# Optimization experiments

Hardware: AMD Instinct MI355X
Metric: run time of the kernel (lower is better)

The kernel has to match this reference:

```python
import jax, jax.numpy as jnp
import numpy as np

ASSIGN_RATIO = 0.1  # hard-coded inside coarsen_graph in the original
EPS_CUT = 1e-7
EPS_NORM = 1e-12  # torch F.normalize eps


def _normalize_batch_adj(adj):
    # adj: [B, N, N]
    n = adj.shape[1]
    A = adj + jnp.eye(n, dtype=adj.dtype)
    deg_inv_sqrt = jnp.clip(A.sum(-1), 1.0, None) ** -0.5  # [B, N]
    newA = deg_inv_sqrt[..., :, None] * A * deg_inv_sqrt[..., None, :]
    row_mask = (adj.sum(-1) > 0).astype(adj.dtype)  # [B, N]
    return row_mask[..., :, None] * newA


def setup_inputs():
    key = jax.random.key(0)
    k0, k1, k2, k3, k4 = jax.random.split(key, 5)
    B, N, D, T = 512, 128, 256, 512
    concept_hidden = jax.random.normal(k0, (B, N, D), jnp.float32)
    adj = jax.random.uniform(k1, (B, N, N), jnp.float32)
    head = jax.random.randint(k2, (B, T), 0, N)
    lin_w = jax.random.normal(k3, (1, D), jnp.float32) / np.sqrt(D).astype(np.float32)
    bias = jax.random.normal(k4, (1,), jnp.float32)
    return {"concept_hidden": concept_hidden, "adj": adj, "head": head,
            "lin_w": lin_w, "bias": bias}


def reference(concept_hidden, adj, head, lin_w, bias):
    # concept_hidden: [B, N, D], adj: [B, N, N], head: [B, T] node indices
    x = concept_hidden
    B, N, D = x.shape

    out = x @ lin_w.T                      # [B, N, 1]  self.lin(x)
    norm_adj = _normalize_batch_adj(adj)   # [B, N, N]
    out = norm_adj @ out + bias            # [B, N, 1]
    alpha = jax.nn.sigmoid(out ** 2)[..., 0]  # [B, N]

    # batch_num_nodes[i] = len(set(head[i]))  -> count unique via sort
    hs = jnp.sort(head, axis=-1)
    n_uniq = 1 + (hs[:, 1:] != hs[:, :-1]).sum(-1)  # [B]

    # per-sample k = ceil(n * 0.1) + 1 (only when n > 1); cut = k-th largest alpha
    k = jnp.ceil(n_uniq.astype(jnp.float32) * ASSIGN_RATIO).astype(jnp.int32) + 1
    a_desc = jnp.sort(alpha, axis=-1)[:, ::-1]       # descending
    idx = jnp.clip(k - 1, 0, N - 1)
    cut = jnp.take_along_axis(a_desc, idx[:, None], axis=-1)[:, 0]
    cut = jnp.where(n_uniq > 1, cut, jnp.zeros_like(cut))  # [B]

    cut_alpha = jax.nn.relu(alpha + EPS_CUT - cut[:, None])  # [B, N]

    # S = norm_adj * cut_alpha broadcast over rows, then L1-normalize rows
    S = norm_adj * cut_alpha[:, None, :]
    S = S / jnp.clip(jnp.abs(S).sum(-1, keepdims=True), EPS_NORM, None)

    St = jnp.swapaxes(S, 1, 2)             # [B, N, N]
    embedding_tensor = St @ x              # S^T x   [B, N, D]
    new_adj = (St @ adj) @ S               # S^T A S [B, N, N]
    return embedding_tensor, new_adj
```

## Files before the change

kernel.cpp:

```cpp
#include <hip/hip_runtime.h>

#define Bsz 512
#define Nn  128
#define Dd  256
#define Tt  512

typedef __attribute__((ext_vector_type(8))) short short8;
typedef __attribute__((ext_vector_type(4))) float f32x4;

__device__ __forceinline__ ushort f2bf(float f) {
    union { float f; unsigned u; } v; v.f = f;
    unsigned r = v.u + 0x7fffu + ((v.u >> 16) & 1u);
    return (ushort)(r >> 16);
}
__device__ __forceinline__ unsigned pk2(float a, float b) {
    return (unsigned)f2bf(a) | ((unsigned)f2bf(b) << 16);
}

__global__ __launch_bounds__(256) void xprep(
    const float* __restrict__ x, const float* __restrict__ lin_w,
    float* __restrict__ dotv2, ushort* __restrict__ xT)
{
    const int h = blockIdx.x, b = blockIdx.y;
    __shared__ float xbufT[32][130];
    __shared__ float pdot[128][8];
    __shared__ float wS[128];
    const int t = threadIdx.x;
    if (t < 128) wS[t] = lin_w[h * 128 + t];
    const int c4 = t & 7;
    const int kb = t >> 3;
    const int kc = t & 15, dsub = t >> 4;
    float p[4] = {0.f, 0.f, 0.f, 0.f};
    __syncthreads();

    for (int c = 0; c < 4; ++c) {
        const int dl = 4 * c4;
        float4 v[4];
#pragma unroll
        for (int i = 0; i < 4; ++i)
            v[i] = *(const float4*)&x[((size_t)b * Nn + (kb + 32 * i)) * Dd
                                      + h * 128 + c * 32 + dl];
        const float w0 = wS[c*32+dl],   w1 = wS[c*32+dl+1];
        const float w2 = wS[c*32+dl+2], w3 = wS[c*32+dl+3];
#pragma unroll
        for (int i = 0; i < 4; ++i) {
            p[i] += v[i].x*w0 + v[i].y*w1 + v[i].z*w2 + v[i].w*w3;
            xbufT[dl    ][kb + 32*i] = v[i].x;
            xbufT[dl + 1][kb + 32*i] = v[i].y;
            xbufT[dl + 2][kb + 32*i] = v[i].z;
            xbufT[dl + 3][kb + 32*i] = v[i].w;
        }
        __syncthreads();
#pragma unroll
        for (int pp = 0; pp < 2; ++pp) {
            int d = dsub + 16 * pp;
            float2 q0 = *(float2*)&xbufT[d][kc*8 + 0];
            float2 q1 = *(float2*)&xbufT[d][kc*8 + 2];
            float2 q2 = *(float2*)&xbufT[d][kc*8 + 4];
            float2 q3 = *(float2*)&xbufT[d][kc*8 + 6];
            uint4 pkv;
            pkv.x = pk2(q0.x, q0.y);
            pkv.y = pk2(q1.x, q1.y);
            pkv.z = pk2(q2.x, q2.y);
            pkv.w = pk2(q3.x, q3.y);
            *(uint4*)&xT[((size_t)b * Dd + h * 128 + c * 32 + d) * Nn + kc * 8] = pkv;
        }
        __syncthreads();
    }
#pragma unroll
    for (int i = 0; i < 4; ++i) pdot[kb + 32*i][c4] = p[i];
    __syncthreads();
    if (t < 128) {
        float s = 0.f;
#pragma unroll
        for (int j = 0; j < 8; ++j) s += pdot[t][j];
        dotv2[((size_t)b * Nn + t) * 2 + h] = s;
    }
}

__global__ __launch_bounds__(256) void sprep(
    const float* __restrict__ adj, const int* __restrict__ head,
    const float* __restrict__ dotv2, const float* __restrict__ bias,
    ushort* __restrict__ STbf)
{
    const int b = blockIdx.x;
    __shared__ __align__(16) float adjS[Nn][132];
    __shared__ __align__(16) float ttS[Nn], disS[Nn], maskS[Nn],
                                   alphaS[Nn], uS[Nn], rowcS[Nn];
    __shared__ float partS[Nn][2];
    __shared__ int   flags[Nn];
    __shared__ int   nuniq_s;
    __shared__ float cut_s;

    const int t = threadIdx.x;
    const float bias0 = bias[0];
    if (t < Nn) flags[t] = 0;
    if (t == 0) { nuniq_s = 0; cut_s = 0.f; }

    const float* adjb = adj + (size_t)b * (Nn * Nn);
#pragma unroll
    for (int i = 0; i < 16; ++i) {
        int f = t + 256 * i;
        int rr = f >> 5, c = (f & 31) * 4;
        *(float4*)&adjS[rr][c] = *(const float4*)&adjb[rr * Nn + c];
    }
    __syncthreads();

    {
        int h0 = head[(size_t)b * Tt + t];
        int h1 = head[(size_t)b * Tt + 256 + t];
        flags[h0] = 1; flags[h1] = 1;
    }

    const int r = t >> 1, hh = t & 1, base = hh * 64;
    {
        float4 s4 = {0.f, 0.f, 0.f, 0.f};
#pragma unroll
        for (int j = 0; j < 16; ++j) {
            float4 v = *(float4*)&adjS[r][base + 4*j];
            s4.x += v.x; s4.y += v.y; s4.z += v.z; s4.w += v.w;
        }
        partS[r][hh] = (s4.x + s4.y) + (s4.z + s4.w);
    }
    __syncthreads();
    if (t < Nn) {
        float rs  = partS[t][0] + partS[t][1];
        float m   = (rs > 0.f) ? 1.f : 0.f;
        float dis = 1.f / sqrtf(fmaxf(rs + 1.f, 1.f));
        maskS[t] = m; disS[t] = dis;
        float lin = dotv2[((size_t)b * Nn + t) * 2]
                  + dotv2[((size_t)b * Nn + t) * 2 + 1];
        ttS[t] = dis * lin;
        atomicAdd(&nuniq_s, flags[t]);
    }
    __syncthreads();
    {
        float4 a = {0.f, 0.f, 0.f, 0.f};
#pragma unroll
        for (int j = 0; j < 16; ++j) {
            float4 v = *(float4*)&adjS[r][base + 4*j];
            float4 w = *(float4*)&ttS[base + 4*j];
            a.x += v.x*w.x; a.y += v.y*w.y; a.z += v.z*w.z; a.w += v.w*w.w;
        }
        partS[r][hh] = (a.x + a.y) + (a.z + a.w);
    }
    __syncthreads();
    if (t < Nn) {
        float mv = partS[t][0] + partS[t][1];
        float o  = maskS[t] * disS[t] * (mv + ttS[t]) + bias0;
        alphaS[t] = 1.f / (1.f + expf(-o * o));
    }
    __syncthreads();
    if (t < Nn) {
        int nu = nuniq_s;
        if (nu > 1) {
            int idx = (int)ceilf((float)nu * 0.1f);
            if (idx > Nn - 1) idx = Nn - 1;
            float an = alphaS[t];
            int cg = 0, ce = 0;
            for (int j = 0; j < Nn; ++j) {
                float aj = alphaS[j];
                cg += (aj > an); ce += (aj == an);
            }
            if (cg <= idx && idx < cg + ce) cut_s = an;
        }
    }
    __syncthreads();
    if (t < Nn) uS[t] = fmaxf(alphaS[t] + 1e-7f - cut_s, 0.f) * disS[t];
    __syncthreads();
    {
        float4 a = {0.f, 0.f, 0.f, 0.f};
#pragma unroll
        for (int j = 0; j < 16; ++j) {
            float4 v = *(float4*)&adjS[r][base + 4*j];
            float4 w = *(float4*)&uS[base + 4*j];
            a.x += v.x*w.x; a.y += v.y*w.y; a.z += v.z*w.z; a.w += v.w*w.w;
        }
        partS[r][hh] = (a.x + a.y) + (a.z + a.w);
    }
    __syncthreads();
    if (t < Nn) {
        float tot  = partS[t][0] + partS[t][1] + uS[t];
        float rsum = maskS[t] * disS[t] * tot;
        rowcS[t] = maskS[t] * disS[t] / fmaxf(rsum, 1e-12f);
    }
    __syncthreads();
    {
        const float um = uS[r];
        ushort* outp = STbf + ((size_t)b * Nn + r) * Nn + base;
#pragma unroll
        for (int kcc = 0; kcc < 8; ++kcc) {
            int k0 = base + kcc * 8;
            float vv[8];
#pragma unroll
            for (int j = 0; j < 8; ++j) {
                int k = k0 + j;
                vv[j] = rowcS[k] * (adjS[k][r] + ((k == r) ? 1.f : 0.f)) * um;
            }
            uint4 pkv;
            pkv.x = pk2(vv[0], vv[1]); pkv.y = pk2(vv[2], vv[3]);
            pkv.z = pk2(vv[4], vv[5]); pkv.w = pk2(vv[6], vv[7]);
            *(uint4*)(outp + kcc * 8) = pkv;
        }
    }
}

__global__ __launch_bounds__(256, 2) void emb_gemm(
    const ushort* __restrict__ STbf, const ushort* __restrict__ xT,
    float* __restrict__ emb)
{
    const int d0 = blockIdx.x * 128;
    const int b  = blockIdx.y;
    __shared__ ushort STl[128][136];
    __shared__ ushort xTl[128][136];
    const int t = threadIdx.x;
    const uint4* sg = (const uint4*)(STbf + (size_t)b * Nn * Nn);
    const uint4* xg = (const uint4*)(xT + ((size_t)b * Dd + d0) * Nn);
#pragma unroll
    for (int i = 0; i < 8; ++i) {
        int f = t + 256 * i;
        int row = f >> 4, c8 = f & 15;
        *(uint4*)&STl[row][c8 * 8] = sg[f];
        *(uint4*)&xTl[row][c8 * 8] = xg[f];
    }
    __syncthreads();

    const int lane = t & 63, wv = t >> 6;
    const int l15 = lane & 15, quad = lane >> 4;
    const int m0 = wv * 32;
    f32x4 acc[2][8];
#pragma unroll
    for (int mt = 0; mt < 2; ++mt)
#pragma unroll
        for (int nt = 0; nt < 8; ++nt) acc[mt][nt] = (f32x4){0.f, 0.f, 0.f, 0.f};

#pragma unroll
    for (int k0 = 0; k0 < 128; k0 += 32) {
        short8 a0 = *(const short8*)&STl[m0 + l15][k0 + quad * 8];
        short8 a1 = *(const short8*)&STl[m0 + 16 + l15][k0 + quad * 8];
        short8 bf[8];
#pragma unroll
        for (int nt = 0; nt < 8; ++nt)
            bf[nt] = *(const short8*)&xTl[nt * 16 + l15][k0 + quad * 8];
#pragma unroll
        for (int nt = 0; nt < 8; ++nt) {
            acc[0][nt] = __builtin_amdgcn_mfma_f32_16x16x32_bf16(a0, bf[nt], acc[0][nt], 0, 0, 0);
            acc[1][nt] = __builtin_amdgcn_mfma_f32_16x16x32_bf16(a1, bf[nt], acc[1][nt], 0, 0, 0);
        }
    }
#pragma unroll
    for (int mt = 0; mt < 2; ++mt)
#pragma unroll
        for (int nt = 0; nt < 8; ++nt)
#pragma unroll
            for (int rr = 0; rr < 4; ++rr) {
                int row = m0 + mt * 16 + quad * 4 + rr;
                int col = d0 + nt * 16 + l15;
                emb[((size_t)b * Nn + row) * Dd + col] = acc[mt][nt][rr];
            }
}

__global__ __launch_bounds__(256, 2) void padj_gemm(
    const float* __restrict__ adj, const ushort* __restrict__ STbf,
    float* __restrict__ nadj)
{
    const int b = blockIdx.x;
    __shared__ ushort bufA[128][136];
    __shared__ ushort STl[128][136];
    const int t = threadIdx.x;

    const float* adjb = adj + (size_t)b * Nn * Nn;
#pragma unroll
    for (int i = 0; i < 16; ++i) {
        int f = t + 256 * i;
        int rr = f >> 5, c4 = f & 31;
        float4 v = *(const float4*)&adjb[rr * Nn + c4 * 4];
        uint2 w; w.x = pk2(v.x, v.y); w.y = pk2(v.z, v.w);
        *(uint2*)&bufA[rr][c4 * 4] = w;
    }
    const uint4* sg = (const uint4*)(STbf + (size_t)b * Nn * Nn);
#pragma unroll
    for (int i = 0; i < 8; ++i) {
        int f = t + 256 * i;
        *(uint4*)&STl[f >> 4][(f & 15) * 8] = sg[f];
    }
    __syncthreads();

    const int lane = t & 63, wv = t >> 6;
    const int l15 = lane & 15, quad = lane >> 4;
    const int m0 = wv * 32;
    f32x4 acc[2][8];
#pragma unroll
    for (int mt = 0; mt < 2; ++mt)
#pragma unroll
        for (int nt = 0; nt < 8; ++nt) acc[mt][nt] = (f32x4){0.f, 0.f, 0.f, 0.f};

#pragma unroll
    for (int k0 = 0; k0 < 128; k0 += 32) {
        short8 a0 = *(const short8*)&bufA[m0 + l15][k0 + quad * 8];
        short8 a1 = *(const short8*)&bufA[m0 + 16 + l15][k0 + quad * 8];
        short8 bf[8];
#pragma unroll
        for (int nt = 0; nt < 8; ++nt)
            bf[nt] = *(const short8*)&STl[nt * 16 + l15][k0 + quad * 8];
#pragma unroll
        for (int nt = 0; nt < 8; ++nt) {
            acc[0][nt] = __builtin_amdgcn_mfma_f32_16x16x32_bf16(a0, bf[nt], acc[0][nt], 0, 0, 0);
            acc[1][nt] = __builtin_amdgcn_mfma_f32_16x16x32_bf16(a1, bf[nt], acc[1][nt], 0, 0, 0);
        }
    }
    __syncthreads();
#pragma unroll
    for (int mt = 0; mt < 2; ++mt)
#pragma unroll
        for (int nt = 0; nt < 8; ++nt) {
            int j    = nt * 16 + l15;
            int mcol = m0 + mt * 16 + quad * 4;
            uint2 w;
            w.x = pk2(acc[mt][nt][0], acc[mt][nt][1]);
            w.y = pk2(acc[mt][nt][2], acc[mt][nt][3]);
            *(uint2*)&bufA[j][mcol] = w;
        }
    __syncthreads();

#pragma unroll
    for (int mt = 0; mt < 2; ++mt)
#pragma unroll
        for (int nt = 0; nt < 8; ++nt) acc[mt][nt] = (f32x4){0.f, 0.f, 0.f, 0.f};

#pragma unroll
    for (int k0 = 0; k0 < 128; k0 += 32) {
        short8 a0 = *(const short8*)&STl[m0 + l15][k0 + quad * 8];
        short8 a1 = *(const short8*)&STl[m0 + 16 + l15][k0 + quad * 8];
        short8 bf[8];
#pragma unroll
        for (int nt = 0; nt < 8; ++nt)
            bf[nt] = *(const short8*)&bufA[nt * 16 + l15][k0 + quad * 8];
#pragma unroll
        for (int nt = 0; nt < 8; ++nt) {
            acc[0][nt] = __builtin_amdgcn_mfma_f32_16x16x32_bf16(a0, bf[nt], acc[0][nt], 0, 0, 0);
            acc[1][nt] = __builtin_amdgcn_mfma_f32_16x16x32_bf16(a1, bf[nt], acc[1][nt], 0, 0, 0);
        }
    }
#pragma unroll
    for (int mt = 0; mt < 2; ++mt)
#pragma unroll
        for (int nt = 0; nt < 8; ++nt)
#pragma unroll
            for (int rr = 0; rr < 4; ++rr) {
                int row = m0 + mt * 16 + quad * 4 + rr;
                int col = nt * 16 + l15;
                nadj[((size_t)b * Nn + row) * Nn + col] = acc[mt][nt][rr];
            }
}

extern "C" void kernel_launch(void* const* d_in, const int* in_sizes, int n_in,
                              void* d_out, int out_size, void* d_ws, size_t ws_size,
                              hipStream_t stream)
{
    const float* x     = (const float*)d_in[0];
    const float* adj   = (const float*)d_in[1];
    const int*   head  = (const int*)d_in[2];
    const float* lin_w = (const float*)d_in[3];
    const float* bias  = (const float*)d_in[4];

    float* emb  = (float*)d_out;
    float* nadj = emb + (size_t)Bsz * Nn * Dd;

    ushort* STbf = (ushort*)d_ws;
    ushort* xT   = STbf + (size_t)Bsz * Nn * Nn;
    float*  dotv2 = (float*)(xT + (size_t)Bsz * Dd * Nn);

    xprep<<<dim3(2, Bsz), 256, 0, stream>>>(x, lin_w, dotv2, xT);
    sprep<<<Bsz, 256, 0, stream>>>(adj, head, dotv2, bias, STbf);
    emb_gemm<<<dim3(2, Bsz), 256, 0, stream>>>(STbf, xT, emb);
    padj_gemm<<<Bsz, 256, 0, stream>>>(adj, STbf, nadj);
}
```

Baseline: 230.6 us.

## Split S construction across more blocks and merge the two GEMM kernels

The monolithic per-sample sprep kernel is split up. Degree and mask row sums move into the x-prep launch as extra blocks. A lighter alphacut kernel reads adj from global memory instead of staging a 64KB shared tile, and a build_st kernel builds S^T with 4 blocks per sample. The embedding and S^T A S GEMMs are merged into one launch with role-selected blocks. The aim is higher occupancy and parallelism in the S-preparation stage, which previously ran one heavy-LDS block per sample. The cost is extra global round-trips for intermediates and adj being re-read several times.

```diff
diff --git a/kernel.cpp b/kernel.cpp
--- a/kernel.cpp
+++ b/kernel.cpp
@@ -17,142 +17,143 @@
     return (unsigned)f2bf(a) | ((unsigned)f2bf(b) << 16);
 }
 
-__global__ __launch_bounds__(256) void xprep(
-    const float* __restrict__ x, const float* __restrict__ lin_w,
-    float* __restrict__ dotv2, ushort* __restrict__ xT)
-{
-    const int h = blockIdx.x, b = blockIdx.y;
+__global__ __launch_bounds__(256) void prep1(
+    const float* __restrict__ x, const float* __restrict__ adj,
+    const float* __restrict__ lin_w,
+    float* __restrict__ dotv2, ushort* __restrict__ xT,
+    float* __restrict__ disG, float* __restrict__ maskG)
+{
+    const int bx = blockIdx.x, b = blockIdx.y;
+    const int t = threadIdx.x;
     __shared__ float xbufT[32][130];
     __shared__ float pdot[128][8];
     __shared__ float wS[128];
-    const int t = threadIdx.x;
-    if (t < 128) wS[t] = lin_w[h * 128 + t];
-    const int c4 = t & 7;
-    const int kb = t >> 3;
-    const int kc = t & 15, dsub = t >> 4;
-    float p[4] = {0.f, 0.f, 0.f, 0.f};
-    __syncthreads();
-
-    for (int c = 0; c < 4; ++c) {
-        const int dl = 4 * c4;
-        float4 v[4];
-#pragma unroll
-        for (int i = 0; i < 4; ++i)
-            v[i] = *(const float4*)&x[((size_t)b * Nn + (kb + 32 * i)) * Dd
-                                      + h * 128 + c * 32 + dl];
-        const float w0 = wS[c*32+dl],   w1 = wS[c*32+dl+1];
-        const float w2 = wS[c*32+dl+2], w3 = wS[c*32+dl+3];
-#pragma unroll
-        for (int i = 0; i < 4; ++i) {
-            p[i] += v[i].x*w0 + v[i].y*w1 + v[i].z*w2 + v[i].w*w3;
-            xbufT[dl    ][kb + 32*i] = v[i].x;
-            xbufT[dl + 1][kb + 32*i] = v[i].y;
-            xbufT[dl + 2][kb + 32*i] = v[i].z;
-            xbufT[dl + 3][kb + 32*i] = v[i].w;
-        }
-        __syncthreads();
-#pragma unroll
-        for (int pp = 0; pp < 2; ++pp) {
-            int d = dsub + 16 * pp;
-            float2 q0 = *(float2*)&xbufT[d][kc*8 + 0];
-            float2 q1 = *(float2*)&xbufT[d][kc*8 + 2];
-            float2 q2 = *(float2*)&xbufT[d][kc*8 + 4];
-            float2 q3 = *(float2*)&xbufT[d][kc*8 + 6];
-            uint4 pkv;
-            pkv.x = pk2(q0.x, q0.y);
-            pkv.y = pk2(q1.x, q1.y);
-            pkv.z = pk2(q2.x, q2.y);
-            pkv.w = pk2(q3.x, q3.y);
-            *(uint4*)&xT[((size_t)b * Dd + h * 128 + c * 32 + d) * Nn + kc * 8] = pkv;
-        }
-        __syncthreads();
-    }
-#pragma unroll
-    for (int i = 0; i < 4; ++i) pdot[kb + 32*i][c4] = p[i];
-    __syncthreads();
+    __shared__ float red[32][8];
+
+    if (bx < 2) {
+        const int h = bx;
+        if (t < 128) wS[t] = lin_w[h * 128 + t];
+        const int c4 = t & 7;
+        const int kb = t >> 3;
+        const int kc = t & 15, dsub = t >> 4;
+        float p[4] = {0.f, 0.f, 0.f, 0.f};
+        __syncthreads();
+        for (int c = 0; c < 4; ++c) {
+            const int dl = 4 * c4;
+            float4 v[4];
+#pragma unroll
+            for (int i = 0; i < 4; ++i)
+                v[i] = *(const float4*)&x[((size_t)b * Nn + (kb + 32 * i)) * Dd
+                                          + h * 128 + c * 32 + dl];
+            const float w0 = wS[c*32+dl],   w1 = wS[c*32+dl+1];
+            const float w2 = wS[c*32+dl+2], w3 = wS[c*32+dl+3];
+#pragma unroll
+            for (int i = 0; i < 4; ++i) {
+                p[i] += v[i].x*w0 + v[i].y*w1 + v[i].z*w2 + v[i].w*w3;
+                xbufT[dl    ][kb + 32*i] = v[i].x;
+                xbufT[dl + 1][kb + 32*i] = v[i].y;
+                xbufT[dl + 2][kb + 32*i] = v[i].z;
+                xbufT[dl + 3][kb + 32*i] = v[i].w;
+            }
+            __syncthreads();
+#pragma unroll
+            for (int pp = 0; pp < 2; ++pp) {
+                int d = dsub + 16 * pp;
+                float2 q0 = *(float2*)&xbufT[d][kc*8 + 0];
+                float2 q1 = *(float2*)&xbufT[d][kc*8 + 2];
+                float2 q2 = *(float2*)&xbufT[d][kc*8 + 4];
+                float2 q3 = *(float2*)&xbufT[d][kc*8 + 6];
+                uint4 pkv;
+                pkv.x = pk2(q0.x, q0.y);
+                pkv.y = pk2(q1.x, q1.y);
+                pkv.z = pk2(q2.x, q2.y);
+                pkv.w = pk2(q3.x, q3.y);
+                *(uint4*)&xT[((size_t)b * Dd + h * 128 + c * 32 + d) * Nn + kc * 8] = pkv;
+            }
+            __syncthreads();
+        }
+#pragma unroll
+        for (int i = 0; i < 4; ++i) pdot[kb + 32*i][c4] = p[i];
+        __syncthreads();
+        if (t < 128) {
+            float s = 0.f;
+#pragma unroll
+            for (int j = 0; j < 8; ++j) s += pdot[t][j];
+            dotv2[((size_t)b * Nn + t) * 2 + h] = s;
+        }
+    } else {
+        const int g = bx - 2;
+        const int r0 = g * 32;
+        const int row = r0 + (t >> 3), sub = t & 7;
+        const float* rp = adj + (size_t)b * Nn * Nn + (size_t)row * Nn + sub * 4;
+        float4 a4 = {0.f, 0.f, 0.f, 0.f};
+#pragma unroll
+        for (int j = 0; j < 4; ++j) {
+            float4 v = *(const float4*)(rp + j * 32);
+            a4.x += v.x; a4.y += v.y; a4.z += v.z; a4.w += v.w;
+        }
+        red[t >> 3][sub] = (a4.x + a4.y) + (a4.z + a4.w);
+        __syncthreads();
+        if (t < 32) {
+            float s = 0.f;
+#pragma unroll
+            for (int j = 0; j < 8; ++j) s += red[t][j];
+            maskG[(size_t)b * Nn + r0 + t] = (s > 0.f) ? 1.f : 0.f;
+            disG[(size_t)b * Nn + r0 + t]  = 1.f / sqrtf(fmaxf(s + 1.f, 1.f));
+        }
+    }
+}
+
+__global__ __launch_bounds__(256) void alphacut(
+    const float* __restrict__ adj, const int* __restrict__ head,
+    const float* __restrict__ dotv2, const float* __restrict__ disG,
+    const float* __restrict__ maskG, const float* __restrict__ bias,
+    float* __restrict__ uG, float* __restrict__ rowcG)
+{
+    const int b = blockIdx.x, t = threadIdx.x;
+    __shared__ float ttS[128], disS[128], maskS[128], alphaS[128], uS[128];
+    __shared__ float partS[128][2];
+    __shared__ int   flags[128];
+    __shared__ int   nuniq;
+    __shared__ float cutS;
+    const float bias0 = bias[0];
+
+    if (t < 128) flags[t] = 0;
+    if (t == 0) { nuniq = 0; cutS = 0.f; }
+    __syncthreads();
+    { int h0 = head[(size_t)b * Tt + t];
+      int h1 = head[(size_t)b * Tt + 256 + t];
+      flags[h0] = 1; flags[h1] = 1; }
     if (t < 128) {
-        float s = 0.f;
-#pragma unroll
-        for (int j = 0; j < 8; ++j) s += pdot[t][j];
-        dotv2[((size_t)b * Nn + t) * 2 + h] = s;
-    }
-}
-
-__global__ __launch_bounds__(256) void sprep(
-    const float* __restrict__ adj, const int* __restrict__ head,
-    const float* __restrict__ dotv2, const float* __restrict__ bias,
-    ushort* __restrict__ STbf)
-{
-    const int b = blockIdx.x;
-    __shared__ __align__(16) float adjS[Nn][132];
-    __shared__ __align__(16) float ttS[Nn], disS[Nn], maskS[Nn],
-                                   alphaS[Nn], uS[Nn], rowcS[Nn];
-    __shared__ float partS[Nn][2];
-    __shared__ int   flags[Nn];
-    __shared__ int   nuniq_s;
-    __shared__ float cut_s;
-
-    const int t = threadIdx.x;
-    const float bias0 = bias[0];
-    if (t < Nn) flags[t] = 0;
-    if (t == 0) { nuniq_s = 0; cut_s = 0.f; }
-
-    const float* adjb = adj + (size_t)b * (Nn * Nn);
-#pragma unroll
-    for (int i = 0; i < 16; ++i) {
-        int f = t + 256 * i;
-        int rr = f >> 5, c = (f & 31) * 4;
-        *(float4*)&adjS[rr][c] = *(const float4*)&adjb[rr * Nn + c];
-    }
-    __syncthreads();
-
-    {
-        int h0 = head[(size_t)b * Tt + t];
-        int h1 = head[(size_t)b * Tt + 256 + t];
-        flags[h0] = 1; flags[h1] = 1;
-    }
-
-    const int r = t >> 1, hh = t & 1, base = hh * 64;
-    {
-        float4 s4 = {0.f, 0.f, 0.f, 0.f};
-#pragma unroll
-        for (int j = 0; j < 16; ++j) {
-            float4 v = *(float4*)&adjS[r][base + 4*j];
-            s4.x += v.x; s4.y += v.y; s4.z += v.z; s4.w += v.w;
-        }
-        partS[r][hh] = (s4.x + s4.y) + (s4.z + s4.w);
-    }
-    __syncthreads();
-    if (t < Nn) {
-        float rs  = partS[t][0] + partS[t][1];
-        float m   = (rs > 0.f) ? 1.f : 0.f;
-        float dis = 1.f / sqrtf(fmaxf(rs + 1.f, 1.f));
-        maskS[t] = m; disS[t] = dis;
-        float lin = dotv2[((size_t)b * Nn + t) * 2]
-                  + dotv2[((size_t)b * Nn + t) * 2 + 1];
-        ttS[t] = dis * lin;
-        atomicAdd(&nuniq_s, flags[t]);
-    }
-    __syncthreads();
+        float d = disG[(size_t)b * Nn + t];
+        disS[t] = d; maskS[t] = maskG[(size_t)b * Nn + t];
+        ttS[t] = d * (dotv2[((size_t)b * Nn + t) * 2]
+                    + dotv2[((size_t)b * Nn + t) * 2 + 1]);
+    }
+    __syncthreads();
+    if (t < 128) atomicAdd(&nuniq, flags[t]);
+
+    const float* adjb = adj + (size_t)b * Nn * Nn;
+    const int r = t >> 1, hh = t & 1, cb = hh * 64;
     {
         float4 a = {0.f, 0.f, 0.f, 0.f};
 #pragma unroll
         for (int j = 0; j < 16; ++j) {
-            float4 v = *(float4*)&adjS[r][base + 4*j];
-            float4 w = *(float4*)&ttS[base + 4*j];
+            float4 v = *(const float4*)&adjb[(size_t)r * Nn + cb + 4*j];
+            float4 w = *(float4*)&ttS[cb + 4*j];
             a.x += v.x*w.x; a.y += v.y*w.y; a.z += v.z*w.z; a.w += v.w*w.w;
         }
         partS[r][hh] = (a.x + a.y) + (a.z + a.w);
     }
     __syncthreads();
-    if (t < Nn) {
+    if (t < 128) {
         float mv = partS[t][0] + partS[t][1];
         float o  = maskS[t] * disS[t] * (mv + ttS[t]) + bias0;
         alphaS[t] = 1.f / (1.f + expf(-o * o));
     }
     __syncthreads();
-    if (t < Nn) {
-        int nu = nuniq_s;
+    if (t < 128) {
+        int nu = nuniq;
         if (nu > 1) {
             int idx = (int)ceilf((float)nu * 0.1f);
             if (idx > Nn - 1) idx = Nn - 1;
@@ -162,66 +163,111 @@
                 float aj = alphaS[j];
                 cg += (aj > an); ce += (aj == an);
             }
-            if (cg <= idx && idx < cg + ce) cut_s = an;
-        }
-    }
-    __syncthreads();
-    if (t < Nn) uS[t] = fmaxf(alphaS[t] + 1e-7f - cut_s, 0.f) * disS[t];
+            if (cg <= idx && idx < cg + ce) cutS = an;
+        }
+    }
+    __syncthreads();
+    if (t < 128) uS[t] = fmaxf(alphaS[t] + 1e-7f - cutS, 0.f) * disS[t];
     __syncthreads();
     {
         float4 a = {0.f, 0.f, 0.f, 0.f};
 #pragma unroll
         for (int j = 0; j < 16; ++j) {
-            float4 v = *(float4*)&adjS[r][base + 4*j];
-            float4 w = *(float4*)&uS[base + 4*j];
+            float4 v = *(const float4*)&adjb[(size_t)r * Nn + cb + 4*j];
+            float4 w = *(float4*)&uS[cb + 4*j];
             a.x += v.x*w.x; a.y += v.y*w.y; a.z += v.z*w.z; a.w += v.w*w.w;
         }
         partS[r][hh] = (a.x + a.y) + (a.z + a.w);
     }
     __syncthreads();
-    if (t < Nn) {
+    if (t < 128) {
         float tot  = partS[t][0] + partS[t][1] + uS[t];
         float rsum = maskS[t] * disS[t] * tot;
-        rowcS[t] = maskS[t] * disS[t] / fmaxf(rsum, 1e-12f);
-    }
-    __syncthreads();
-    {
-        const float um = uS[r];
-        ushort* outp = STbf + ((size_t)b * Nn + r) * Nn + base;
-#pragma unroll
-        for (int kcc = 0; kcc < 8; ++kcc) {
-            int k0 = base + kcc * 8;
-            float vv[8];
-#pragma unroll
-            for (int j = 0; j < 8; ++j) {
-                int k = k0 + j;
-                vv[j] = rowcS[k] * (adjS[k][r] + ((k == r) ? 1.f : 0.f)) * um;
-            }
-            uint4 pkv;
-            pkv.x = pk2(vv[0], vv[1]); pkv.y = pk2(vv[2], vv[3]);
-            pkv.z = pk2(vv[4], vv[5]); pkv.w = pk2(vv[6], vv[7]);
-            *(uint4*)(outp + kcc * 8) = pkv;
-        }
-    }
-}
-
-__global__ __launch_bounds__(256, 2) void emb_gemm(
-    const ushort* __restrict__ STbf, const ushort* __restrict__ xT,
-    float* __restrict__ emb)
-{
-    const int d0 = blockIdx.x * 128;
-    const int b  = blockIdx.y;
-    __shared__ ushort STl[128][136];
-    __shared__ ushort xTl[128][136];
+        rowcG[(size_t)b * Nn + t] = maskS[t] * disS[t] / fmaxf(rsum, 1e-12f);
+        uG[(size_t)b * Nn + t]    = uS[t];
+    }
+}
+
+__global__ __launch_bounds__(256) void build_st(
+    const float* __restrict__ adj, const float* __restrict__ uG,
+    const float* __restrict__ rowcG, ushort* __restrict__ STbf)
+{
+    const int g = blockIdx.x, b = blockIdx.y, t = threadIdx.x;
+    const int m0 = g * 32;
+    __shared__ float slabT[32][132];
+    __shared__ float rowcS[128];
+    __shared__ float uS[32];
+
+    if (t < 128) rowcS[t] = rowcG[(size_t)b * Nn + t];
+    if (t < 32)  uS[t]    = uG[(size_t)b * Nn + m0 + t];
+
+    const float* adjb = adj + (size_t)b * Nn * Nn;
+#pragma unroll
+    for (int i = 0; i < 4; ++i) {
+        int f = t + 256 * i;
+        int k = f >> 3, cc = (f & 7) * 4;
+        float4 v = *(const float4*)&adjb[(size_t)k * Nn + m0 + cc];
+        slabT[cc    ][k] = v.x; slabT[cc + 1][k] = v.y;
+        slabT[cc + 2][k] = v.z; slabT[cc + 3][k] = v.w;
+    }
+    __syncthreads();
+
+    const int mloc = t >> 3, m = m0 + mloc;
+    const int ks   = (t & 7) * 16;
+    const float um = uS[mloc];
+    float vv[16];
+#pragma unroll
+    for (int q = 0; q < 4; ++q) {
+        float4 a = *(float4*)&slabT[mloc][ks + 4 * q];
+        int k = ks + 4 * q;
+        vv[4*q    ] = rowcS[k    ] * (a.x + ((k     == m) ? 1.f : 0.f)) * um;
+        vv[4*q + 1] = rowcS[k + 1] * (a.y + ((k + 1 == m) ? 1.f : 0.f)) * um;
+        vv[4*q + 2] = rowcS[k + 2] * (a.z + ((k + 2 == m) ? 1.f : 0.f)) * um;
+        vv[4*q + 3] = rowcS[k + 3] * (a.w + ((k + 3 == m) ? 1.f : 0.f)) * um;
+    }
+    uint4 p0, p1;
+    p0.x = pk2(vv[0],  vv[1]);  p0.y = pk2(vv[2],  vv[3]);
+    p0.z = pk2(vv[4],  vv[5]);  p0.w = pk2(vv[6],  vv[7]);
+    p1.x = pk2(vv[8],  vv[9]);  p1.y = pk2(vv[10], vv[11]);
+    p1.z = pk2(vv[12], vv[13]); p1.w = pk2(vv[14], vv[15]);
+    ushort* outp = STbf + ((size_t)b * Nn + m) * Nn + ks;
+    *(uint4*)outp       = p0;
+    *(uint4*)(outp + 8) = p1;
+}
+
+__global__ __launch_bounds__(256, 2) void gemm3(
+    const float* __restrict__ adj, const ushort* __restrict__ STbf,
+    const ushort* __restrict__ xT, float* __restrict__ emb,
+    float* __restrict__ nadj)
+{
+    const int role = blockIdx.x, b = blockIdx.y;
+    __shared__ ushort bufB[128][136];
+    __shared__ ushort bufS[128][136];
     const int t = threadIdx.x;
+
     const uint4* sg = (const uint4*)(STbf + (size_t)b * Nn * Nn);
-    const uint4* xg = (const uint4*)(xT + ((size_t)b * Dd + d0) * Nn);
 #pragma unroll
     for (int i = 0; i < 8; ++i) {
         int f = t + 256 * i;
-        int row = f >> 4, c8 = f & 15;
-        *(uint4*)&STl[row][c8 * 8] = sg[f];
-        *(uint4*)&xTl[row][c8 * 8] = xg[f];
+        *(uint4*)&bufS[f >> 4][(f & 15) * 8] = sg[f];
+    }
+    if (role < 2) {
+        const uint4* xg = (const uint4*)(xT + ((size_t)b * Dd + role * 128) * Nn);
+#pragma unroll
+        for (int i = 0; i < 8; ++i) {
+            int f = t + 256 * i;
+            *(uint4*)&bufB[f >> 4][(f & 15) * 8] = xg[f];
+        }
+    } else {
+        const float* adjb = adj + (size_t)b * Nn * Nn;
+#pragma unroll
+        for (int i = 0; i < 16; ++i) {
+            int f = t + 256 * i;
+            int rr = f >> 5, c4 = f & 31;
+            float4 v = *(const float4*)&adjb[(size_t)rr * Nn + c4 * 4];
+            uint2 w; w.x = pk2(v.x, v.y); w.y = pk2(v.z, v.w);
+            *(uint2*)&bufB[rr][c4 * 4] = w;
+        }
     }
     __syncthreads();
 
@@ -234,124 +280,89 @@
 #pragma unroll
         for (int nt = 0; nt < 8; ++nt) acc[mt][nt] = (f32x4){0.f, 0.f, 0.f, 0.f};
 
-#pragma unroll
-    for (int k0 = 0; k0 < 128; k0 += 32) {
-        short8 a0 = *(const short8*)&STl[m0 + l15][k0 + quad * 8];
-        short8 a1 = *(const short8*)&STl[m0 + 16 + l15][k0 + quad * 8];
-        short8 bf[8];
-#pragma unroll
-        for (int nt = 0; nt < 8; ++nt)
-            bf[nt] = *(const short8*)&xTl[nt * 16 + l15][k0 + quad * 8];
-#pragma unroll
-        for (int nt = 0; nt < 8; ++nt) {
-            acc[0][nt] = __builtin_amdgcn_mfma_f32_16x16x32_bf16(a0, bf[nt], acc[0][nt], 0, 0, 0);
-            acc[1][nt] = __builtin_amdgcn_mfma_f32_16x16x32_bf16(a1, bf[nt], acc[1][nt], 0, 0, 0);
-        }
-    }
-#pragma unroll
-    for (int mt = 0; mt < 2; ++mt)
-#pragma unroll
-        for (int nt = 0; nt < 8; ++nt)
-#pragma unroll
-            for (int rr = 0; rr < 4; ++rr) {
-                int row = m0 + mt * 16 + quad * 4 + rr;
-                int col = d0 + nt * 16 + l15;
-                emb[((size_t)b * Nn + row) * Dd + col] = acc[mt][nt][rr];
-            }
-}
-
-__global__ __launch_bounds__(256, 2) void padj_gemm(
-    const float* __restrict__ adj, const ushort* __restrict__ STbf,
-    float* __restrict__ nadj)
-{
-    const int b = blockIdx.x;
-    __shared__ ushort bufA[128][136];
-    __shared__ ushort STl[128][136];
-    const int t = threadIdx.x;
-
-    const float* adjb = adj + (size_t)b * Nn * Nn;
-#pragma unroll
-    for (int i = 0; i < 16; ++i) {
-        int f = t + 256 * i;
-        int rr = f >> 5, c4 = f & 31;
-        float4 v = *(const float4*)&adjb[rr * Nn + c4 * 4];
-        uint2 w; w.x = pk2(v.x, v.y); w.y = pk2(v.z, v.w);
-        *(uint2*)&bufA[rr][c4 * 4] = w;
-    }
-    const uint4* sg = (const uint4*)(STbf + (size_t)b * Nn * Nn);
-#pragma unroll
-    for (int i = 0; i < 8; ++i) {
-        int f = t + 256 * i;
-        *(uint4*)&STl[f >> 4][(f & 15) * 8] = sg[f];
-    }
-    __syncthreads();
-
-    const int lane = t & 63, wv = t >> 6;
-    const int l15 = lane & 15, quad = lane >> 4;
-    const int m0 = wv * 32;
-    f32x4 acc[2][8];
-#pragma unroll
-    for (int mt = 0; mt < 2; ++mt)
-#pragma unroll
-        for (int nt = 0; nt < 8; ++nt) acc[mt][nt] = (f32x4){0.f, 0.f, 0.f, 0.f};
-
-#pragma unroll
-    for (int k0 = 0; k0 < 128; k0 += 32) {
-        short8 a0 = *(const short8*)&bufA[m0 + l15][k0 + quad * 8];
-        short8 a1 = *(const short8*)&bufA[m0 + 16 + l15][k0 + quad * 8];
-        short8 bf[8];
-#pragma unroll
-        for (int nt = 0; nt < 8; ++nt)
-            bf[nt] = *(const short8*)&STl[nt * 16 + l15][k0 + quad * 8];
-#pragma unroll
-        for (int nt = 0; nt < 8; ++nt) {
-            acc[0][nt] = __builtin_amdgcn_mfma_f32_16x16x32_bf16(a0, bf[nt], acc[0][nt], 0, 0, 0);
-            acc[1][nt] = __builtin_amdgcn_mfma_f32_16x16x32_bf16(a1, bf[nt], acc[1][nt], 0, 0, 0);
-        }
-    }
-    __syncthreads();
-#pragma unroll
-    for (int mt = 0; mt < 2; ++mt)
-#pragma unroll
-        for (int nt = 0; nt < 8; ++nt) {
-            int j    = nt * 16 + l15;
-            int mcol = m0 + mt * 16 + quad * 4;
-            uint2 w;
-            w.x = pk2(acc[mt][nt][0], acc[mt][nt][1]);
-            w.y = pk2(acc[mt][nt][2], acc[mt][nt][3]);
-            *(uint2*)&bufA[j][mcol] = w;
-        }
-    __syncthreads();
-
-#pragma unroll
-    for (int mt = 0; mt < 2; ++mt)
-#pragma unroll
-        for (int nt = 0; nt < 8; ++nt) acc[mt][nt] = (f32x4){0.f, 0.f, 0.f, 0.f};
-
-#pragma unroll
-    for (int k0 = 0; k0 < 128; k0 += 32) {
-        short8 a0 = *(const short8*)&STl[m0 + l15][k0 + quad * 8];
-        short8 a1 = *(const short8*)&STl[m0 + 16 + l15][k0 + quad * 8];
-        short8 bf[8];
-#pragma unroll
-        for (int nt = 0; nt < 8; ++nt)
-            bf[nt] = *(const short8*)&bufA[nt * 16 + l15][k0 + quad * 8];
-#pragma unroll
-        for (int nt = 0; nt < 8; ++nt) {
-            acc[0][nt] = __builtin_amdgcn_mfma_f32_16x16x32_bf16(a0, bf[nt], acc[0][nt], 0, 0, 0);
-            acc[1][nt] = __builtin_amdgcn_mfma_f32_16x16x32_bf16(a1, bf[nt], acc[1][nt], 0, 0, 0);
-        }
-    }
-#pragma unroll
-    for (int mt = 0; mt < 2; ++mt)
-#pragma unroll
-        for (int nt = 0; nt < 8; ++nt)
-#pragma unroll
-            for (int rr = 0; rr < 4; ++rr) {
-                int row = m0 + mt * 16 + quad * 4 + rr;
-                int col = nt * 16 + l15;
-                nadj[((size_t)b * Nn + row) * Nn + col] = acc[mt][nt][rr];
-            }
+    if (role < 2) {
+#pragma unroll
+        for (int k0 = 0; k0 < 128; k0 += 32) {
+            short8 a0 = *(const short8*)&bufS[m0 + l15][k0 + quad * 8];
+            short8 a1 = *(const short8*)&bufS[m0 + 16 + l15][k0 + quad * 8];
+            short8 bf[8];
+#pragma unroll
+            for (int nt = 0; nt < 8; ++nt)
+                bf[nt] = *(const short8*)&bufB[nt * 16 + l15][k0 + quad * 8];
+#pragma unroll
+            for (int nt = 0; nt < 8; ++nt) {
+                acc[0][nt] = __builtin_amdgcn_mfma_f32_16x16x32_bf16(a0, bf[nt], acc[0][nt], 0, 0, 0);
+                acc[1][nt] = __builtin_amdgcn_mfma_f32_16x16x32_bf16(a1, bf[nt], acc[1][nt], 0, 0, 0);
+            }
+        }
+        const int d0 = role * 128;
+#pragma unroll
+        for (int mt = 0; mt < 2; ++mt)
+#pragma unroll
+            for (int nt = 0; nt < 8; ++nt)
+#pragma unroll
+                for (int rr = 0; rr < 4; ++rr) {
+                    int row = m0 + mt * 16 + quad * 4 + rr;
+                    int col = d0 + nt * 16 + l15;
+                    emb[((size_t)b * Nn + row) * Dd + col] = acc[mt][nt][rr];
+                }
+    } else {
+#pragma unroll
+        for (int k0 = 0; k0 < 128; k0 += 32) {
+            short8 a0 = *(const short8*)&bufB[m0 + l15][k0 + quad * 8];
+            short8 a1 = *(const short8*)&bufB[m0 + 16 + l15][k0 + quad * 8];
+            short8 bf[8];
+#pragma unroll
+            for (int nt = 0; nt < 8; ++nt)
+                bf[nt] = *(const short8*)&bufS[nt * 16 + l15][k0 + quad * 8];
+#pragma unroll
+            for (int nt = 0; nt < 8; ++nt) {
+                acc[0][nt] = __builtin_amdgcn_mfma_f32_16x16x32_bf16(a0, bf[nt], acc[0][nt], 0, 0, 0);
+                acc[1][nt] = __builtin_amdgcn_mfma_f32_16x16x32_bf16(a1, bf[nt], acc[1][nt], 0, 0, 0);
+            }
+        }
+        __syncthreads();
+#pragma unroll
+        for (int mt = 0; mt < 2; ++mt)
+#pragma unroll
+            for (int nt = 0; nt < 8; ++nt) {
+                int j    = nt * 16 + l15;
+                int mcol = m0 + mt * 16 + quad * 4;
+                uint2 w;
+                w.x = pk2(acc[mt][nt][0], acc[mt][nt][1]);
+                w.y = pk2(acc[mt][nt][2], acc[mt][nt][3]);
+                *(uint2*)&bufB[j][mcol] = w;
+            }
+        __syncthreads();
+#pragma unroll
+        for (int mt = 0; mt < 2; ++mt)
+#pragma unroll
+            for (int nt = 0; nt < 8; ++nt) acc[mt][nt] = (f32x4){0.f, 0.f, 0.f, 0.f};
+#pragma unroll
+        for (int k0 = 0; k0 < 128; k0 += 32) {
+            short8 a0 = *(const short8*)&bufS[m0 + l15][k0 + quad * 8];
+            short8 a1 = *(const short8*)&bufS[m0 + 16 + l15][k0 + quad * 8];
+            short8 bf[8];
+#pragma unroll
+            for (int nt = 0; nt < 8; ++nt)
+                bf[nt] = *(const short8*)&bufB[nt * 16 + l15][k0 + quad * 8];
+#pragma unroll
+            for (int nt = 0; nt < 8; ++nt) {
+                acc[0][nt] = __builtin_amdgcn_mfma_f32_16x16x32_bf16(a0, bf[nt], acc[0][nt], 0, 0, 0);
+                acc[1][nt] = __builtin_amdgcn_mfma_f32_16x16x32_bf16(a1, bf[nt], acc[1][nt], 0, 0, 0);
+            }
+        }
+#pragma unroll
+        for (int mt = 0; mt < 2; ++mt)
+#pragma unroll
+            for (int nt = 0; nt < 8; ++nt)
+#pragma unroll
+                for (int rr = 0; rr < 4; ++rr) {
+                    int row = m0 + mt * 16 + quad * 4 + rr;
+                    int col = nt * 16 + l15;
+                    nadj[((size_t)b * Nn + row) * Nn + col] = acc[mt][nt][rr];
+                }
+    }
 }
 
 extern "C" void kernel_launch(void* const* d_in, const int* in_sizes, int n_in,
@@ -367,12 +378,16 @@
     float* emb  = (float*)d_out;
     float* nadj = emb + (size_t)Bsz * Nn * Dd;
 
-    ushort* STbf = (ushort*)d_ws;
-    ushort* xT   = STbf + (size_t)Bsz * Nn * Nn;
+    ushort* STbf  = (ushort*)d_ws;
+    ushort* xT    = STbf + (size_t)Bsz * Nn * Nn;
     float*  dotv2 = (float*)(xT + (size_t)Bsz * Dd * Nn);
-
-    xprep<<<dim3(2, Bsz), 256, 0, stream>>>(x, lin_w, dotv2, xT);
-    sprep<<<Bsz, 256, 0, stream>>>(adj, head, dotv2, bias, STbf);
-    emb_gemm<<<dim3(2, Bsz), 256, 0, stream>>>(STbf, xT, emb);
-    padj_gemm<<<Bsz, 256, 0, stream>>>(adj, STbf, nadj);
-}
+    float*  disG  = dotv2 + (size_t)Bsz * Nn * 2;
+    float*  maskG = disG + (size_t)Bsz * Nn;
+    float*  uG    = maskG + (size_t)Bsz * Nn;
+    float*  rowcG = uG + (size_t)Bsz * Nn;
+
+    prep1<<<dim3(6, Bsz), 256, 0, stream>>>(x, adj, lin_w, dotv2, xT, disG, maskG);
+    alphacut<<<Bsz, 256, 0, stream>>>(adj, head, dotv2, disG, maskG, bias, uG, rowcG);
+    build_st<<<dim3(4, Bsz), 256, 0, stream>>>(adj, uG, rowcG, STbf);
+    gemm3<<<dim3(3, Bsz), 256, 0, stream>>>(adj, STbf, xT, emb, nadj);
+}
```

New measurement: 232.2 us. No clear change (+0.7%).
